# Optimization experiments

Measured on AMD Instinct MI355X. Metric: run time of the kernel, lower is better.

Reference implementation:

```python
import jax, jax.numpy as jnp
import numpy as np

CAPACITY = 60.0
CONS_RATE = 0.2
T_LIMIT = 11.0
VELOCITY = 60.0
NUM_AFS = 3
BS, SEQ, H = 256, 256, 128
NEG = -1e9


def setup_inputs() -> dict:
    key = jax.random.key(0)
    ks = jax.random.split(key, 12)
    coords = jax.random.uniform(ks[0], (BS, SEQ, 2))
    static = jnp.transpose(coords, (0, 2, 1))  # [bs, 2, seq]
    diff = coords[:, :, None, :] - coords[:, None, :, :]
    distances = jnp.sqrt(jnp.sum(diff * diff, -1) + 1e-12)  # [bs, seq, seq]
    demands = jax.random.uniform(ks[1], (BS, SEQ), minval=0.1, maxval=1.0)
    demands = demands.at[:, :NUM_AFS + 1].set(0.0)  # depot + AFS have no demand
    dynamic = jnp.stack([jnp.full((BS, SEQ), CAPACITY),
                         jnp.full((BS, SEQ), T_LIMIT),
                         demands], axis=1)  # [bs, 3, seq]
    p = lambda k, shape: 0.1 * jax.random.normal(k, shape)
    return dict(
        static=static, dynamic=dynamic, distances=distances,
        W_s=p(ks[2], (H, 2)), b_s=jnp.zeros(H),
        W_d=p(ks[3], (H, 3)), b_d=jnp.zeros(H),
        W_i=p(ks[4], (4 * H, H)), W_h=p(ks[5], (4 * H, H)),
        b_i=jnp.zeros(4 * H), b_h=jnp.zeros(4 * H),
        W_att=p(ks[6], (H, 3 * H)), v_att=p(ks[7], (H,)),
        W_c=p(ks[8], (H, 2 * H)), b_c=jnp.zeros(H),
        decode_steps=128)


def reference(static, dynamic, distances, W_s, b_s, W_d, b_d, W_i, W_h, b_i, b_h,
              W_att, v_att, W_c, b_c, decode_steps):
    bs, _, seq = static.shape
    h = W_s.shape[0]
    arange_b = jnp.arange(bs)
    node_ids = jnp.arange(seq)

    # Encoder = Conv1d(kernel=1): [bs,c,seq] -> [bs,h,seq]
    stat_emb = jnp.einsum('oc,bcs->bos', W_s, static) + b_s[None, :, None]

    # dis_by_afs: cheapest via-AFS distance from each node to depot
    dba = jnp.stack([distances[:, i, 0:1] + distances[:, i, :]
                     for i in range(1, NUM_AFS + 1)], 1)  # [bs, num_afs, seq]
    dis_by_afs = jnp.min(dba, axis=1).at[:, 0].set(0.0)    # [bs, seq]

    fuel0 = dynamic[:, 0, 0]
    time0 = dynamic[:, 1, 0]
    dem0 = dynamic[:, 2, :]
    ones_seq = jnp.ones((1, seq), static.dtype)

    def enc_dyn(fuel, time, dem):
        dyn = jnp.stack([fuel[:, None] * ones_seq, time[:, None] * ones_seq, dem], 1)
        return jnp.einsum('oc,bcs->bos', W_d, dyn) + b_d[None, :, None]

    def step(carry, key):
        fuel, time, dem, hst, cst, old_idx, dec_in, mask = carry
        dyn_emb = enc_dyn(fuel, time, dem)
        # one LSTM step (PyTorch gate order i,f,g,o)
        gates = dec_in @ W_i.T + hst @ W_h.T + b_i + b_h
        ig, fg, gg, og = jnp.split(gates, 4, axis=-1)
        cst = jax.nn.sigmoid(fg) * cst + jax.nn.sigmoid(ig) * jnp.tanh(gg)
        h_lstm = jax.nn.sigmoid(og) * jnp.tanh(cst)
        # pointer attention over nodes
        feat = jnp.concatenate(
            [stat_emb, dyn_emb, jnp.broadcast_to(h_lstm[:, :, None], (bs, h, seq))], axis=1)
        e = jnp.einsum('k,bks->bs', v_att,
                       jnp.tanh(jnp.einsum('kc,bcs->bks', W_att, feat)))
        logits = jnp.where(mask, e, NEG)
        idx = jax.random.categorical(key, logits)               # sample next node
        logp = jax.nn.log_softmax(logits)[arange_b, idx]
        probs = jax.nn.softmax(logits)
        context = jnp.einsum('bs,bhs->bh', probs, stat_emb)
        h_new = jnp.tanh(jnp.concatenate([context, h_lstm], -1) @ W_c.T + b_c)
        # update_fn: fuel/time/demand dynamics + feasibility mask
        dis = distances[arange_b, old_idx, idx]
        fuel = fuel - CONS_RATE * dis
        time = time - dis / VELOCITY
        at_dep = idx == 0
        at_af = (idx >= 1) & (idx <= NUM_AFS)
        fuel = jnp.where(at_dep | at_af, CAPACITY, fuel)
        time = jnp.where(at_dep, T_LIMIT, time)
        dem = dem.at[arange_b, idx].set(jnp.where(idx > NUM_AFS, 0.0, dem[arange_b, idx]))
        d_next = distances[arange_b, idx, :]  # [bs, seq]
        fuel_ok = fuel[:, None] >= CONS_RATE * (d_next + dis_by_afs)
        time_ok = time[:, None] >= (d_next + distances[:, :, 0]) / VELOCITY
        cust_mask = (dem > 0) & fuel_ok & time_ok
        depot_af_mask = node_ids[None, :] != idx[:, None]
        mask = jnp.where(node_ids[None, :] <= NUM_AFS, depot_af_mask, cust_mask)
        mask = mask.at[:, 0].set(True)  # depot always reachable -> no all-masked rows
        dec_in = stat_emb[arange_b, :, idx]
        return (fuel, time, dem, h_new, cst, idx, dec_in, mask), (probs, idx, logp)

    init = (fuel0, time0, dem0,
            jnp.zeros((bs, h)), jnp.zeros((bs, h)),
            jnp.zeros(bs, jnp.int32), stat_emb[:, :, 0],
            jnp.ones((bs, seq), bool))
    keys = jax.random.split(jax.random.key(1), decode_steps)
    _, (probs, tours, logps) = jax.lax.scan(step, init, keys)
    # outputs [bs, T, seq], tours [bs, T], tour_logp [bs, T]
    return jnp.transpose(probs, (1, 0, 2)), tours.T, logps.T
```

## Files before the change

kernel.cpp:

```cpp
#include <hip/hip_runtime.h>
#include <cmath>

#define BSZ 256
#define SEQN 256
#define HD 128
#define NEGV -1000000000.0f
#define TINYF 1.17549435e-38f
#define LOG2E 1.4426950408889634f
#define LN2F 0.6931471805599453f

typedef float v2f __attribute__((ext_vector_type(2)));

static __device__ __forceinline__ v2f mk2(float a, float b) {
  v2f r; r.x = a; r.y = b; return r;
}
static __device__ __forceinline__ v2f fma2(v2f a, v2f b, v2f c) {
  return __builtin_elementwise_fma(a, b, c);
}

static __device__ __forceinline__ void tf2x32(unsigned k0, unsigned k1,
                                              unsigned x0, unsigned x1,
                                              unsigned &o0, unsigned &o1) {
  unsigned ks2 = k0 ^ k1 ^ 0x1BD11BDAu;
#define TFR(r) { x0 += x1; x1 = (x1 << (r)) | (x1 >> (32 - (r))); x1 ^= x0; }
  x0 += k0; x1 += k1;
  TFR(13) TFR(15) TFR(26) TFR(6)
  x0 += k1; x1 += ks2 + 1u;
  TFR(17) TFR(29) TFR(16) TFR(24)
  x0 += ks2; x1 += k0 + 2u;
  TFR(13) TFR(15) TFR(26) TFR(6)
  x0 += k0; x1 += k1 + 3u;
  TFR(17) TFR(29) TFR(16) TFR(24)
  x0 += k1; x1 += ks2 + 4u;
  TFR(13) TFR(15) TFR(26) TFR(6)
  x0 += ks2; x1 += k0 + 5u;
#undef TFR
  o0 = x0; o1 = x1;
}

static __device__ __forceinline__ float fast_tanh(float x) {
  float y = __fmul_rn(x, 2.885390081777927f);
  float ay = __int_as_float(__float_as_int(y) | 0x80000000u);
  float q = __builtin_amdgcn_exp2f(ay);
  float r = __fmul_rn(__fsub_rn(1.0f, q),
                      __builtin_amdgcn_rcpf(__fadd_rn(1.0f, q)));
  unsigned sgn = (unsigned)__float_as_int(x) & 0x80000000u;
  return __int_as_float(__float_as_int(r) | sgn);
}

static __device__ __forceinline__ float fast_sig(float x) {
  float q = __builtin_amdgcn_exp2f(__fmul_rn(x, -LOG2E));
  return __builtin_amdgcn_rcpf(__fadd_rn(1.0f, q));
}

static __device__ __forceinline__ float fast_ln(float x) {
  return __fmul_rn(__builtin_amdgcn_logf(x), LN2F);
}

static __device__ __forceinline__ v2f tanh2(v2f x) {
  v2f y = x * mk2(2.885390081777927f, 2.885390081777927f);
  y = __builtin_elementwise_min(y, mk2(48.0f, 48.0f));
  v2f s; s.x = __builtin_amdgcn_exp2f(y.x); s.y = __builtin_amdgcn_exp2f(y.y);
  v2f n = s + mk2(-1.0f, -1.0f);
  v2f d = s + mk2(1.0f, 1.0f);
  v2f r; r.x = __builtin_amdgcn_rcpf(d.x); r.y = __builtin_amdgcn_rcpf(d.y);
  return n * r;
}

__global__ __launch_bounds__(512, 2) void evrp_kernel(
    const float* __restrict__ statc, const float* __restrict__ dyn,
    const float* __restrict__ dist,  const float* __restrict__ W_s,
    const float* __restrict__ b_s,   const float* __restrict__ W_d,
    const float* __restrict__ b_d,   const float* __restrict__ W_i,
    const float* __restrict__ W_h,   const float* __restrict__ b_i,
    const float* __restrict__ b_h,   const float* __restrict__ W_att,
    const float* __restrict__ v_att, const float* __restrict__ W_c,
    const float* __restrict__ b_c,   const int* __restrict__ steps_p,
    float* __restrict__ out) {
  const int b = blockIdx.x;
  const int tid = threadIdx.x;
  const int T = steps_p[0];
  const int lane = tid & 63;
  const int wv = tid >> 6;
  const int s = tid >> 1, hf = tid & 1;
  const int cq = tid >> 2, g = tid & 3;

  extern __shared__ __align__(16) float4 Pdyn[];

  __shared__ __align__(16) float  B0a[HD], B1a[HD], A2a[HD];
  __shared__ __align__(16) float  Ct[HD], Vt[HD];
  __shared__ __align__(16) float  hstm[HD], hlm[HD], wc2v[HD];
  __shared__ __align__(16) float  A0a[HD], A1a[HD], D0a[HD];
  __shared__ __align__(16) float  C0a[HD], C1a[HD], C2a[HD], bca[HD];
  __shared__ __align__(16) float2 xy2[SEQN];
  __shared__ __align__(16) float  drowX[SEQN];
  __shared__ __align__(16) unsigned kAs[256], kBs[256];
  __shared__ __align__(16) float ws0[HD], ws1[HD], bsv[HD];
  __shared__ __align__(16) float wd0[HD], wd1[HD], wd2[HD], bdv[HD];
  __shared__ float rv[8], rS[8], rpx[8], rpy[8];
  __shared__ int ri[8];

  const float* distb = dist + (size_t)b * SEQN * SEQN;

  if (tid < HD) {
    ws0[tid] = W_s[2 * tid]; ws1[tid] = W_s[2 * tid + 1]; bsv[tid] = b_s[tid];
    wd0[tid] = W_d[3 * tid]; wd1[tid] = W_d[3 * tid + 1]; wd2[tid] = W_d[3 * tid + 2];
    bdv[tid] = b_d[tid]; bca[tid] = b_c[tid];
    hstm[tid] = 0.0f;
  }
  float xreg = statc[b * 2 * SEQN + s];
  float yreg = statc[b * 2 * SEQN + SEQN + s];
  float demreg = dyn[b * 3 * SEQN + 2 * SEQN + s];
  float d2dR = distb[(size_t)s * SEQN];
  float dbaR;
  {
    float d10 = distb[1 * SEQN + 0], d20 = distb[2 * SEQN + 0], d30 = distb[3 * SEQN + 0];
    float d1s = distb[1 * SEQN + s], d2s = distb[2 * SEQN + s], d3s = distb[3 * SEQN + s];
    float m = fminf(fminf(__fadd_rn(d10, d1s), __fadd_rn(d20, d2s)), __fadd_rn(d30, d3s));
    dbaR = (s == 0) ? 0.0f : m;
  }
  float dnextR = distb[s];
  if (hf == 0) xy2[s] = make_float2(xreg, yreg);
  float fuelR = dyn[b * 3 * SEQN + 0];
  float timeR = dyn[b * 3 * SEQN + SEQN + 0];
  float cstR = 0.0f;
  int niR = 0;
  for (int tt = tid; tt < 256; tt += 512) {
    unsigned a0, a1; tf2x32(0u, 1u, 0u, (unsigned)tt, a0, a1);
    kAs[tt] = a0; kBs[tt] = a1;
  }
  __syncthreads();

  if (tid < HD) {
    int k = tid;
    const float* row = W_att + (size_t)k * 384;
    float B0 = 0, B1 = 0, B2 = 0, A0 = 0, A1 = 0, A2 = 0, A3 = 0;
    for (int c = 0; c < HD; ++c) {
      float w1 = row[c], w2 = row[128 + c];
      B0 = fmaf(w1, ws0[c], B0); B1 = fmaf(w1, ws1[c], B1); B2 = fmaf(w1, bsv[c], B2);
      A0 = fmaf(w2, wd0[c], A0); A1 = fmaf(w2, wd1[c], A1);
      A2 = fmaf(w2, wd2[c], A2); A3 = fmaf(w2, bdv[c], A3);
    }
    B0a[k] = B0; B1a[k] = B1; A2a[k] = A2; Vt[k] = v_att[k];
    A0a[k] = A0; A1a[k] = A1; D0a[k] = __fadd_rn(B2, A3);
  } else if (tid < 2 * HD) {
    int o = tid - HD;
    const float* row = W_c + (size_t)o * 256;
    float C0 = 0, C1 = 0, C2 = 0;
    for (int c = 0; c < HD; ++c) {
      float w = row[c];
      C0 = fmaf(w, ws0[c], C0); C1 = fmaf(w, ws1[c], C1); C2 = fmaf(w, bsv[c], C2);
    }
    C0a[o] = C0; C1a[o] = C1; C2a[o] = C2;
  }
  float gp0 = 0, gp1 = 0, gp2 = 0, gpw;
  {
    int j = g * HD + cq;
    const float* row = W_i + (size_t)j * HD;
    for (int c = 0; c < HD; ++c) {
      float w = row[c];
      gp0 = fmaf(w, ws0[c], gp0); gp1 = fmaf(w, ws1[c], gp1); gp2 = fmaf(w, bsv[c], gp2);
    }
    gpw = __fadd_rn(b_i[j], b_h[j]);
  }
  v2f whreg2[HD / 2];
  {
    int j = g * HD + cq;
#pragma unroll
    for (int c2 = 0; c2 < HD / 2; ++c2)
      whreg2[c2] = *(const v2f*)(&W_h[(size_t)j * HD + 2 * c2]);
  }
  v2f wah2[16], wc22[16];
#pragma unroll
  for (int i = 0; i < 16; ++i) {
    wah2[i] = *(const v2f*)(&W_att[(size_t)cq * 384 + 256 + g * 32 + 2 * i]);
    wc22[i] = *(const v2f*)(&W_c[(size_t)cq * 256 + HD + g * 32 + 2 * i]);
  }
#pragma unroll
  for (int c = 0; c < HD / 2; c += 2)
    asm volatile("" : "+v"(whreg2[c]), "+v"(whreg2[c + 1]));
#pragma unroll
  for (int i = 0; i < 16; i += 2) {
    asm volatile("" : "+v"(wah2[i]), "+v"(wah2[i + 1]));
    asm volatile("" : "+v"(wc22[i]), "+v"(wc22[i + 1]));
  }
  __syncthreads();

  for (int idx = tid; idx < SEQN * HD; idx += 512) {
    int ss = idx >> 7, k = idx & 127;
    float2 pxy = xy2[ss];
    float dm = dyn[b * 3 * SEQN + 2 * SEQN + ss];
    float pv = fmaf(B0a[k], pxy.x, fmaf(B1a[k], pxy.y, __fmul_rn(A2a[k], dm)));
    ((float*)Pdyn)[(((k >> 2) & 15) << 11) + ((ss * 2 + (k >> 6)) << 2) + (k & 3)] = pv;
  }
  __syncthreads();

  float decxR = xy2[0].x, decyR = xy2[0].y;

  float* out_probs = out;
  float* out_tours = out + (size_t)BSZ * T * SEQN;
  float* out_logps = out_tours + (size_t)BSZ * T;

  const float4* Pp = Pdyn + (s * 2 + hf);
  const float* CtH = Ct + hf * 64;
  const float* VtH = Vt + hf * 64;

  for (int t = 0; t < T; ++t) {
    {
      v2f mA = mk2(0.f, 0.f), mB = mk2(0.f, 0.f);
      const float4* h4 = (const float4*)hstm;
#pragma unroll
      for (int c4 = 0; c4 < HD / 4; ++c4) {
        float4 hh = h4[c4];
        mA = fma2(whreg2[2 * c4],     mk2(hh.x, hh.y), mA);
        mB = fma2(whreg2[2 * c4 + 1], mk2(hh.z, hh.w), mB);
      }
      float md = fmaf(gp0, decxR, fmaf(gp1, decyR, gp2));
      float mh = __fadd_rn(__fadd_rn(mA.x, mA.y), __fadd_rn(mB.x, mB.y));
      float V = __fadd_rn(__fadd_rn(md, mh), gpw);
      float sg = fast_sig(V), th = fast_tanh(V);
      float q = (g == 2) ? th : sg;
      float u1 = __shfl_xor(q, 1, 64);
      float u2 = __shfl_xor(q, 2, 64);
      float u3 = __shfl_xor(q, 3, 64);
      float qi = (g == 0) ? q  : (g == 1) ? u1 : (g == 2) ? u2 : u3;
      float qf = (g == 0) ? u1 : (g == 1) ? q  : (g == 2) ? u3 : u2;
      float qg = (g == 0) ? u2 : (g == 1) ? u3 : (g == 2) ? q  : u1;
      float qo = (g == 0) ? u3 : (g == 1) ? u2 : (g == 2) ? u1 : q;
      float cn = __fadd_rn(__fmul_rn(qf, cstR), __fmul_rn(qi, qg));
      cstR = cn;
      float hv = __fmul_rn(qo, fast_tanh(cn));
      if (g == 0) hlm[(cq & 96) | ((cq & 31) ^ ((cq >> 5) << 3))] = hv;
    }
    __syncthreads();
    {
      v2f pwA = mk2(0.f, 0.f), pwB = mk2(0.f, 0.f);
      v2f pcA = mk2(0.f, 0.f), pcB = mk2(0.f, 0.f);
      const float4* hl4 = (const float4*)hlm;
#pragma unroll
      for (int l4 = 0; l4 < 8; ++l4) {
        float4 hh = hl4[(g << 3) + (l4 ^ (g << 1))];
        v2f hA = mk2(hh.x, hh.y), hB = mk2(hh.z, hh.w);
        pwA = fma2(wah2[2 * l4],     hA, pwA);
        pwB = fma2(wah2[2 * l4 + 1], hB, pwB);
        pcA = fma2(wc22[2 * l4],     hA, pcA);
        pcB = fma2(wc22[2 * l4 + 1], hB, pcB);
      }
      float pw = __fadd_rn(__fadd_rn(pwA.x, pwA.y), __fadd_rn(pwB.x, pwB.y));
      float pc = __fadd_rn(__fadd_rn(pcA.x, pcA.y), __fadd_rn(pcB.x, pcB.y));
      pw = __fadd_rn(pw, __shfl_xor(pw, 1, 64));
      pc = __fadd_rn(pc, __shfl_xor(pc, 1, 64));
      pw = __fadd_rn(pw, __shfl_xor(pw, 2, 64));
      pc = __fadd_rn(pc, __shfl_xor(pc, 2, 64));
      if (g == 0) {
        wc2v[cq] = pc;
        Ct[cq] = fmaf(A0a[cq], fuelR, fmaf(A1a[cq], timeR, __fadd_rn(D0a[cq], pw)));
      }
    }
    __syncthreads();
    float pe, lg;
    if (hf == 0) drowX[s] = dnextR;
    bool mk;
    if (t == 0) mk = true;
    else {
      bool fok = fuelR >= __fmul_rn(0.2f, __fadd_rn(dnextR, dbaR));
      bool tok = timeR >= __fdiv_rn(__fadd_rn(dnextR, d2dR), 60.0f);
      bool cust = (demreg > 0.0f) && fok && tok;
      mk = (s <= 3) ? (s != niR) : cust;
      if (s == 0) mk = true;
    }
    {
      unsigned rb;
      { unsigned o0, o1; tf2x32(kAs[t], kBs[t], 0u, (unsigned)(b * SEQN + s), o0, o1); rb = o0 ^ o1; }
      float f = __uint_as_float((rb >> 9) | 0x3f800000u) - 1.0f;
      float u = fmaxf(TINYF, __fadd_rn(f, TINYF));
      float gmb = -fast_ln(-fast_ln(u));
      v2f acc2 = mk2(0.f, 0.f);
#pragma unroll
      for (int i = 0; i < 16; ++i) {
        float4 pv = Pp[i << 9];
        float4 ct = *(const float4*)(CtH + 4 * i);
        float4 vv = *(const float4*)(VtH + 4 * i);
        v2f a0 = mk2(pv.x, pv.y) + mk2(ct.x, ct.y);
        acc2 = fma2(mk2(vv.x, vv.y), tanh2(a0), acc2);
        v2f a1 = mk2(pv.z, pv.w) + mk2(ct.z, ct.w);
        acc2 = fma2(mk2(vv.z, vv.w), tanh2(a1), acc2);
      }
      float acc = __fadd_rn(acc2.x, acc2.y);
      float e = __fadd_rn(acc, __shfl_xor(acc, 1, 64));
      lg = mk ? e : NEGV;
      pe = __builtin_amdgcn_exp2f(__fmul_rn(lg, LOG2E));
      float sc = __fadd_rn(gmb, lg);
      float av = sc; int ai = s;
      float S = pe, px = __fmul_rn(pe, xreg), py = __fmul_rn(pe, yreg);
#pragma unroll
      for (int off = 2; off < 64; off <<= 1) {
        float ov = __shfl_xor(av, off, 64);
        int   oi = __shfl_xor(ai, off, 64);
        if (ov > av || (ov == av && oi < ai)) { av = ov; ai = oi; }
        S  = __fadd_rn(S,  __shfl_xor(S,  off, 64));
        px = __fadd_rn(px, __shfl_xor(px, off, 64));
        py = __fadd_rn(py, __shfl_xor(py, off, 64));
      }
      if (lane == 0) { rv[wv] = av; ri[wv] = ai; rS[wv] = S; rpx[wv] = px; rpy[wv] = py; }
    }
    __syncthreads();
    {
      float bv = rv[0]; int bi = ri[0];
#pragma unroll
      for (int w = 1; w < 8; ++w)
        if (rv[w] > bv) { bv = rv[w]; bi = ri[w]; }
      int ni = bi;
      dnextR = distb[(size_t)ni * SEQN + s];
      float S = rS[0], px = rpx[0], py = rpy[0];
#pragma unroll
      for (int w = 1; w < 8; ++w) {
        S = __fadd_rn(S, rS[w]); px = __fadd_rn(px, rpx[w]); py = __fadd_rn(py, rpy[w]);
      }
      float dis = drowX[ni];
      float fl = __fsub_rn(fuelR, __fmul_rn(0.2f, dis));
      float tm = __fsub_rn(timeR, __fdiv_rn(dis, 60.0f));
      if (ni <= 3) fl = 60.0f;
      if (ni == 0) tm = 11.0f;
      fuelR = fl; timeR = tm;
      if (s == ni && ni > 3) demreg = 0.0f;
      float2 dxy = xy2[ni];
      decxR = dxy.x; decyR = dxy.y;
      float pr = __fdiv_rn(pe, S);
      if (hf == 0) out_probs[((size_t)b * T + t) * SEQN + s] = pr;
      if (s == ni && hf == 0) {
        out_tours[(size_t)b * T + t] = (float)ni;
        out_logps[(size_t)b * T + t] = __fsub_rn(lg, fast_ln(S));
      }
      if (tid < HD) {
        float cx = __fdiv_rn(px, S), cy = __fdiv_rn(py, S);
        float ctxd = fmaf(C0a[tid], cx, fmaf(C1a[tid], cy, C2a[tid]));
        float val = __fadd_rn(__fadd_rn(ctxd, wc2v[tid]), bca[tid]);
        hstm[tid] = fast_tanh(val);
      }
      niR = ni;
    }
    __syncthreads();
  }
}

extern "C" void kernel_launch(void* const* d_in, const int* in_sizes, int n_in,
                              void* d_out, int out_size, void* d_ws, size_t ws_size,
                              hipStream_t stream) {
  (void)in_sizes; (void)n_in; (void)out_size; (void)d_ws; (void)ws_size;
  (void)hipFuncSetAttribute((const void*)evrp_kernel,
                            hipFuncAttributeMaxDynamicSharedMemorySize,
                            SEQN * HD * 4);
  evrp_kernel<<<dim3(BSZ), dim3(512), SEQN * HD * 4, stream>>>(
      (const float*)d_in[0],  (const float*)d_in[1],  (const float*)d_in[2],
      (const float*)d_in[3],  (const float*)d_in[4],  (const float*)d_in[5],
      (const float*)d_in[6],  (const float*)d_in[7],  (const float*)d_in[8],
      (const float*)d_in[9],  (const float*)d_in[10], (const float*)d_in[11],
      (const float*)d_in[12], (const float*)d_in[13], (const float*)d_in[14],
      (const int*)d_in[15],   (float*)d_out);
}
```

Before: 930.3 us.

## Use DPP/swizzle wave reductions and defer output stores and dist loads

Replaces the ds_bpermute-based __shfl_xor reductions inside quads and within each wave with DPP quad permutes, row shifts and ds_swizzle. Only the cross-half xor-32 step still uses a shuffle. The per-wave partials are packed into float2/float4 shared arrays so the cross-wave combine needs fewer LDS reads. Global stores of probs, tour and logp, plus the next distance-row load, are moved to the start of the following step so they overlap with the LSTM compute instead of sitting on the critical path before the barrier. This adds registers for the carried values and depends on the DPP row_shr patterns giving correct xor-equivalent reductions.

```diff
diff --git a/kernel.cpp b/kernel.cpp
--- a/kernel.cpp
+++ b/kernel.cpp
@@ -17,6 +17,10 @@
 static __device__ __forceinline__ v2f fma2(v2f a, v2f b, v2f c) {
   return __builtin_elementwise_fma(a, b, c);
 }
+
+#define DPPF(x, c) __int_as_float(__builtin_amdgcn_update_dpp(0, __float_as_int(x), (c), 0xF, 0xF, true))
+#define DPPI(x, c) __builtin_amdgcn_update_dpp(0, (x), (c), 0xF, 0xF, true)
+#define SWZF(x, p) __int_as_float(__builtin_amdgcn_ds_swizzle(__float_as_int(x), (p)))
 
 static __device__ __forceinline__ void tf2x32(unsigned k0, unsigned k1,
                                               unsigned x0, unsigned x1,
@@ -97,8 +101,8 @@
   __shared__ __align__(16) unsigned kAs[256], kBs[256];
   __shared__ __align__(16) float ws0[HD], ws1[HD], bsv[HD];
   __shared__ __align__(16) float wd0[HD], wd1[HD], wd2[HD], bdv[HD];
-  __shared__ float rv[8], rS[8], rpx[8], rpy[8];
-  __shared__ int ri[8];
+  __shared__ __align__(16) float2 wredA[8];
+  __shared__ __align__(16) float4 wredB[8];
 
   const float* distb = dist + (size_t)b * SEQN * SEQN;
 
@@ -205,7 +209,18 @@
   const float* CtH = Ct + hf * 64;
   const float* VtH = Vt + hf * 64;
 
+  float prevPr = 0.0f, prevLp = 0.0f;
+  int prevNi = 0;
+
   for (int t = 0; t < T; ++t) {
+    if (t > 0) {
+      if (hf == 0) out_probs[((size_t)b * T + (t - 1)) * SEQN + s] = prevPr;
+      if (s == prevNi && hf == 0) {
+        out_tours[(size_t)b * T + (t - 1)] = (float)prevNi;
+        out_logps[(size_t)b * T + (t - 1)] = prevLp;
+      }
+      dnextR = distb[(size_t)niR * SEQN + s];
+    }
     {
       v2f mA = mk2(0.f, 0.f), mB = mk2(0.f, 0.f);
       const float4* h4 = (const float4*)hstm;
@@ -220,9 +235,9 @@
       float V = __fadd_rn(__fadd_rn(md, mh), gpw);
       float sg = fast_sig(V), th = fast_tanh(V);
       float q = (g == 2) ? th : sg;
-      float u1 = __shfl_xor(q, 1, 64);
-      float u2 = __shfl_xor(q, 2, 64);
-      float u3 = __shfl_xor(q, 3, 64);
+      float u1 = DPPF(q, 0xB1);
+      float u2 = DPPF(q, 0x4E);
+      float u3 = DPPF(q, 0x1B);
       float qi = (g == 0) ? q  : (g == 1) ? u1 : (g == 2) ? u2 : u3;
       float qf = (g == 0) ? u1 : (g == 1) ? q  : (g == 2) ? u3 : u2;
       float qg = (g == 0) ? u2 : (g == 1) ? u3 : (g == 2) ? q  : u1;
@@ -248,10 +263,10 @@
       }
       float pw = __fadd_rn(__fadd_rn(pwA.x, pwA.y), __fadd_rn(pwB.x, pwB.y));
       float pc = __fadd_rn(__fadd_rn(pcA.x, pcA.y), __fadd_rn(pcB.x, pcB.y));
-      pw = __fadd_rn(pw, __shfl_xor(pw, 1, 64));
-      pc = __fadd_rn(pc, __shfl_xor(pc, 1, 64));
-      pw = __fadd_rn(pw, __shfl_xor(pw, 2, 64));
-      pc = __fadd_rn(pc, __shfl_xor(pc, 2, 64));
+      pw = __fadd_rn(pw, DPPF(pw, 0xB1));
+      pc = __fadd_rn(pc, DPPF(pc, 0xB1));
+      pw = __fadd_rn(pw, DPPF(pw, 0x4E));
+      pc = __fadd_rn(pc, DPPF(pc, 0x4E));
       if (g == 0) {
         wc2v[cq] = pc;
         Ct[cq] = fmaf(A0a[cq], fuelR, fmaf(A1a[cq], timeR, __fadd_rn(D0a[cq], pw)));
@@ -287,35 +302,68 @@
         acc2 = fma2(mk2(vv.z, vv.w), tanh2(a1), acc2);
       }
       float acc = __fadd_rn(acc2.x, acc2.y);
-      float e = __fadd_rn(acc, __shfl_xor(acc, 1, 64));
+      float e = __fadd_rn(acc, DPPF(acc, 0xB1));
       lg = mk ? e : NEGV;
       pe = __builtin_amdgcn_exp2f(__fmul_rn(lg, LOG2E));
       float sc = __fadd_rn(gmb, lg);
       float av = sc; int ai = s;
       float S = pe, px = __fmul_rn(pe, xreg), py = __fmul_rn(pe, yreg);
-#pragma unroll
-      for (int off = 2; off < 64; off <<= 1) {
-        float ov = __shfl_xor(av, off, 64);
-        int   oi = __shfl_xor(ai, off, 64);
+      {
+        float ov = DPPF(av, 0x4E); int oi = DPPI(ai, 0x4E);
         if (ov > av || (ov == av && oi < ai)) { av = ov; ai = oi; }
-        S  = __fadd_rn(S,  __shfl_xor(S,  off, 64));
-        px = __fadd_rn(px, __shfl_xor(px, off, 64));
-        py = __fadd_rn(py, __shfl_xor(py, off, 64));
-      }
-      if (lane == 0) { rv[wv] = av; ri[wv] = ai; rS[wv] = S; rpx[wv] = px; rpy[wv] = py; }
+        S  = __fadd_rn(S,  DPPF(S,  0x4E));
+        px = __fadd_rn(px, DPPF(px, 0x4E));
+        py = __fadd_rn(py, DPPF(py, 0x4E));
+      }
+      {
+        float ov = DPPF(av, 0x124); int oi = DPPI(ai, 0x124);
+        if (ov > av || (ov == av && oi < ai)) { av = ov; ai = oi; }
+        S  = __fadd_rn(S,  DPPF(S,  0x124));
+        px = __fadd_rn(px, DPPF(px, 0x124));
+        py = __fadd_rn(py, DPPF(py, 0x124));
+      }
+      {
+        float ov = DPPF(av, 0x128); int oi = DPPI(ai, 0x128);
+        if (ov > av || (ov == av && oi < ai)) { av = ov; ai = oi; }
+        S  = __fadd_rn(S,  DPPF(S,  0x128));
+        px = __fadd_rn(px, DPPF(px, 0x128));
+        py = __fadd_rn(py, DPPF(py, 0x128));
+      }
+      {
+        float ov = SWZF(av, 0x401F); int oi = __builtin_amdgcn_ds_swizzle(ai, 0x401F);
+        if (ov > av || (ov == av && oi < ai)) { av = ov; ai = oi; }
+        S  = __fadd_rn(S,  SWZF(S,  0x401F));
+        px = __fadd_rn(px, SWZF(px, 0x401F));
+        py = __fadd_rn(py, SWZF(py, 0x401F));
+      }
+      {
+        float ov = __shfl_xor(av, 32, 64); int oi = __shfl_xor(ai, 32, 64);
+        if (ov > av || (ov == av && oi < ai)) { av = ov; ai = oi; }
+        S  = __fadd_rn(S,  __shfl_xor(S,  32, 64));
+        px = __fadd_rn(px, __shfl_xor(px, 32, 64));
+        py = __fadd_rn(py, __shfl_xor(py, 32, 64));
+      }
+      if (lane == 0) {
+        wredA[wv] = make_float2(av, (float)ai);
+        wredB[wv] = make_float4(S, px, py, 0.0f);
+      }
     }
     __syncthreads();
     {
-      float bv = rv[0]; int bi = ri[0];
-#pragma unroll
-      for (int w = 1; w < 8; ++w)
-        if (rv[w] > bv) { bv = rv[w]; bi = ri[w]; }
+      float2 a0 = wredA[0];
+      float bv = a0.x; int bi = (int)a0.y;
+#pragma unroll
+      for (int w = 1; w < 8; ++w) {
+        float2 aw = wredA[w];
+        if (aw.x > bv) { bv = aw.x; bi = (int)aw.y; }
+      }
       int ni = bi;
-      dnextR = distb[(size_t)ni * SEQN + s];
-      float S = rS[0], px = rpx[0], py = rpy[0];
+      float4 b0 = wredB[0];
+      float S = b0.x, px = b0.y, py = b0.z;
 #pragma unroll
       for (int w = 1; w < 8; ++w) {
-        S = __fadd_rn(S, rS[w]); px = __fadd_rn(px, rpx[w]); py = __fadd_rn(py, rpy[w]);
+        float4 bw = wredB[w];
+        S = __fadd_rn(S, bw.x); px = __fadd_rn(px, bw.y); py = __fadd_rn(py, bw.z);
       }
       float dis = drowX[ni];
       float fl = __fsub_rn(fuelR, __fmul_rn(0.2f, dis));
@@ -326,12 +374,9 @@
       if (s == ni && ni > 3) demreg = 0.0f;
       float2 dxy = xy2[ni];
       decxR = dxy.x; decyR = dxy.y;
-      float pr = __fdiv_rn(pe, S);
-      if (hf == 0) out_probs[((size_t)b * T + t) * SEQN + s] = pr;
-      if (s == ni && hf == 0) {
-        out_tours[(size_t)b * T + t] = (float)ni;
-        out_logps[(size_t)b * T + t] = __fsub_rn(lg, fast_ln(S));
-      }
+      prevPr = __fdiv_rn(pe, S);
+      prevLp = __fsub_rn(lg, fast_ln(S));
+      prevNi = ni;
       if (tid < HD) {
         float cx = __fdiv_rn(px, S), cy = __fdiv_rn(py, S);
         float ctxd = fmaf(C0a[tid], cx, fmaf(C1a[tid], cy, C2a[tid]));
@@ -341,6 +386,11 @@
       niR = ni;
     }
     __syncthreads();
+  }
+  if (hf == 0) out_probs[((size_t)b * T + (T - 1)) * SEQN + s] = prevPr;
+  if (s == prevNi && hf == 0) {
+    out_tours[(size_t)b * T + (T - 1)] = (float)prevNi;
+    out_logps[(size_t)b * T + (T - 1)] = prevLp;
   }
 }
 
```

After: 853.2 us. -8.3%, faster.
